# Performance work log

Hardware: AMD Instinct MI355X
Metric: run time of the kernel (lower is better)

The kernel has to match this reference:

```python
import jax, jax.numpy as jnp
import numpy as np

N = 50000
E = 800000
F_IN = 128
HID = 128
H_HID = 4
H_OUT = 6
N_CLS = 40
NEG_SLOPE = 0.2
BN_EPS = 1e-5


def gat_conv(x, src, dst, W, a_src, a_dst, bias, concat):
    # x: [N, F_in]; W: [F_in, H*C]; a_src/a_dst: [H, C]
    H, C = a_src.shape
    h = (x @ W).reshape(N, H, C)                      # [N,H,C]
    alpha_s = jnp.sum(h * a_src[None], axis=-1)       # [N,H]
    alpha_d = jnp.sum(h * a_dst[None], axis=-1)       # [N,H]
    e = jax.nn.leaky_relu(alpha_s[src] + alpha_d[dst], NEG_SLOPE)  # [E',H]
    # segment softmax over incoming edges of each dst node
    emax = jax.ops.segment_max(e, dst, num_segments=N)
    e = jnp.exp(e - emax[dst])
    denom = jax.ops.segment_sum(e, dst, num_segments=N)
    alpha = e / (denom[dst] + 1e-16)                  # [E',H]
    out = jax.ops.segment_sum(alpha[:, :, None] * h[src], dst, num_segments=N)  # [N,H,C]
    out = out.reshape(N, H * C) if concat else out.mean(axis=1)
    return out + bias


def bn_eval(x, gamma, beta, mean, var):
    return (x - mean) * (gamma / jnp.sqrt(var + BN_EPS)) + beta


def setup_inputs() -> dict:
    key = jax.random.key(0)
    ks = jax.random.split(key, 24)
    d_h = HID * H_HID  # 512
    inp = {
        'x': jax.random.normal(ks[0], (N, F_IN), jnp.float32),
        'edge_index': jax.random.randint(ks[1], (2, E), 0, N, jnp.int64),
        # layer 0: GATConv(128 -> 128, heads=4, concat)
        'W0': jax.random.normal(ks[2], (F_IN, d_h), jnp.float32) * 0.1,
        'as0': jax.random.normal(ks[3], (H_HID, HID), jnp.float32) * 0.1,
        'ad0': jax.random.normal(ks[4], (H_HID, HID), jnp.float32) * 0.1,
        'b0': jnp.zeros((d_h,), jnp.float32),
        'g0': jax.random.uniform(ks[5], (d_h,), jnp.float32, 0.5, 1.5),
        'bt0': jax.random.normal(ks[6], (d_h,), jnp.float32) * 0.1,
        'm0': jax.random.normal(ks[7], (d_h,), jnp.float32) * 0.1,
        'v0': jax.random.uniform(ks[8], (d_h,), jnp.float32, 0.5, 1.5),
        # layer 1: GATConv(512 -> 128, heads=4, concat)
        'W1': jax.random.normal(ks[9], (d_h, d_h), jnp.float32) * 0.05,
        'as1': jax.random.normal(ks[10], (H_HID, HID), jnp.float32) * 0.1,
        'ad1': jax.random.normal(ks[11], (H_HID, HID), jnp.float32) * 0.1,
        'b1': jnp.zeros((d_h,), jnp.float32),
        'g1': jax.random.uniform(ks[12], (d_h,), jnp.float32, 0.5, 1.5),
        'bt1': jax.random.normal(ks[13], (d_h,), jnp.float32) * 0.1,
        'm1': jax.random.normal(ks[14], (d_h,), jnp.float32) * 0.1,
        'v1': jax.random.uniform(ks[15], (d_h,), jnp.float32, 0.5, 1.5),
        # layer 2: GATConv(512 -> 40, heads=6, concat=False)
        'W2': jax.random.normal(ks[16], (d_h, H_OUT * N_CLS), jnp.float32) * 0.05,
        'as2': jax.random.normal(ks[17], (H_OUT, N_CLS), jnp.float32) * 0.1,
        'ad2': jax.random.normal(ks[18], (H_OUT, N_CLS), jnp.float32) * 0.1,
        'b2': jnp.zeros((N_CLS,), jnp.float32),
    }
    return inp


def reference(x, edge_index, W0, as0, ad0, b0, g0, bt0, m0, v0,
              W1, as1, ad1, b1, g1, bt1, m1, v1,
              W2, as2, ad2, b2):
    # add self loops (PyG GATConv default add_self_loops=True)
    loop = jnp.arange(N, dtype=edge_index.dtype)
    src = jnp.concatenate([edge_index[0], loop])
    dst = jnp.concatenate([edge_index[1], loop])
    # dropout is a no-op in eval mode
    h = gat_conv(x, src, dst, W0, as0, ad0, b0, concat=True)
    h = jax.nn.elu(bn_eval(h, g0, bt0, m0, v0))
    h = gat_conv(h, src, dst, W1, as1, ad1, b1, concat=True)
    h = jax.nn.elu(bn_eval(h, g1, bt1, m1, v1))
    h = gat_conv(h, src, dst, W2, as2, ad2, b2, concat=False)
    return jax.nn.log_softmax(h, axis=-1)
```

## Files before the change

### kernel.cpp

```cpp
#include <hip/hip_runtime.h>
#include <cstdint>
#include <cstddef>

#define NN 50000
#define EE 800000
#define EPQ (EE + NN)
#define NEG_SLOPE 0.2f
#define BN_EPS 1e-5f
#define SCB 256
#define NBLK ((NN + SCB - 1) / SCB)

typedef _Float16 f16x8 __attribute__((ext_vector_type(8)));
typedef _Float16 f16x4 __attribute__((ext_vector_type(4)));
typedef _Float16 f16x2 __attribute__((ext_vector_type(2)));
typedef float f32x4 __attribute__((ext_vector_type(4)));
typedef float f32x2 __attribute__((ext_vector_type(2)));
typedef unsigned int u32;
typedef unsigned char u8;
typedef unsigned short u16;

static __device__ __forceinline__ float lrelu(float x) { return x > 0.f ? x : x * NEG_SLOPE; }

static __device__ __forceinline__ u8 f32_to_fp8(float v) {
    return (u8)(__builtin_amdgcn_cvt_pk_fp8_f32(v, v, 0, false) & 0xff);
}
static __device__ __forceinline__ void fp8x4_to_f32(u32 v, float* o) {
    f32x2 lo = __builtin_amdgcn_cvt_pk_f32_fp8(v, false);
    f32x2 hi = __builtin_amdgcn_cvt_pk_f32_fp8(v, true);
    o[0] = lo[0]; o[1] = lo[1]; o[2] = hi[0]; o[3] = hi[1];
}

static __device__ __forceinline__ void gld_lds16(const void* g, void* l) {
    __builtin_amdgcn_global_load_lds((const __attribute__((address_space(1))) u32*)g,
                                     (__attribute__((address_space(3))) u32*)l, 16, 0, 0);
}

__global__ void hist_kernel(const int* __restrict__ dst, int* __restrict__ count) {
    int e = blockIdx.x * blockDim.x + threadIdx.x;
    if (e < EE) atomicAdd(&count[dst[e]], 1);
}

__global__ __launch_bounds__(SCB) void scan1(const int* __restrict__ count,
                                             int* __restrict__ excl, int* __restrict__ bsum) {
    __shared__ int tmp[SCB];
    int b = blockIdx.x, t = threadIdx.x;
    int i = b * SCB + t;
    int v = (i < NN) ? count[i] + 1 : 0;
    tmp[t] = v;
    __syncthreads();
    for (int off = 1; off < SCB; off <<= 1) {
        int u = (t >= off) ? tmp[t - off] : 0;
        __syncthreads();
        tmp[t] += u;
        __syncthreads();
    }
    if (i < NN) excl[i] = tmp[t] - v;
    if (t == SCB - 1) bsum[b] = tmp[t];
}

__global__ __launch_bounds__(256) void scan2(const int* __restrict__ bsum, int* __restrict__ boff) {
    __shared__ int tmp[256];
    int t = threadIdx.x;
    int v = (t < NBLK) ? bsum[t] : 0;
    tmp[t] = v;
    __syncthreads();
    for (int off = 1; off < 256; off <<= 1) {
        int u = (t >= off) ? tmp[t - off] : 0;
        __syncthreads();
        tmp[t] += u;
        __syncthreads();
    }
    boff[t] = tmp[t] - v;
}

__global__ void scan3(const int* __restrict__ excl, const int* __restrict__ boff,
                      int* __restrict__ rowptr, int* __restrict__ cursor) {
    int i = blockIdx.x * blockDim.x + threadIdx.x;
    if (i < NN) {
        int r = excl[i] + boff[i / SCB];
        rowptr[i] = r;
        cursor[i] = r;
    }
    if (i == NN) rowptr[NN] = EPQ;
}

__global__ void scatter_kernel(const int* __restrict__ src, const int* __restrict__ dst,
                               int* __restrict__ cursor, int* __restrict__ csrs) {
    int e = blockIdx.x * blockDim.x + threadIdx.x;
    if (e < EE) {
        int d = dst[e];
        int slot = atomicAdd(&cursor[d], 1);
        csrs[slot] = src[e];
    } else if (e < EPQ) {
        int i = e - EE;
        int slot = atomicAdd(&cursor[i], 1);
        csrs[slot] = i;
    }
}

__global__ __launch_bounds__(256) void tcast_all(const float* __restrict__ W0,
                                                 const float* __restrict__ W1,
                                                 const float* __restrict__ W2,
                                                 _Float16* __restrict__ W0t,
                                                 _Float16* __restrict__ W1t,
                                                 _Float16* __restrict__ W2t) {
    __shared__ float tile[32][33];
    int b = blockIdx.x;
    const float* W; _Float16* Wt; int K, Nc, bx, by;
    if (b < 64)       { W = W0; Wt = W0t; K = 128; Nc = 512; int q = b;       bx = q % 16, by = q / 16; }
    else if (b < 320) { W = W1; Wt = W1t; K = 512; Nc = 512; int q = b - 64;  bx = q % 16, by = q / 16; }
    else              { W = W2; Wt = W2t; K = 512; Nc = 240; int q = b - 320; bx = q % 8,  by = q / 8; }
    bx *= 32; by *= 32;
    int tx = threadIdx.x & 31, ty = threadIdx.x >> 5;
#pragma unroll
    for (int r = 0; r < 32; r += 8) {
        int k = by + ty + r, n = bx + tx;
        tile[ty + r][tx] = (k < K && n < Nc) ? W[(size_t)k * Nc + n] : 0.f;
    }
    __syncthreads();
#pragma unroll
    for (int r = 0; r < 32; r += 8) {
        int n = bx + ty + r, k = by + tx;
        if (n < Nc && k < K) Wt[(size_t)n * K + k] = (_Float16)tile[tx][ty + r];
    }
}

__global__ __launch_bounds__(1024) void prep_all(const float* g0, const float* bt0,
                                                 const float* m0, const float* v0, const float* b0,
                                                 const float* g1, const float* bt1,
                                                 const float* m1, const float* v1, const float* b1,
                                                 const _Float16* __restrict__ W0t,
                                                 const _Float16* __restrict__ W1t,
                                                 const _Float16* __restrict__ W2t,
                                                 const float* __restrict__ as0,
                                                 const float* __restrict__ ad0,
                                                 const float* __restrict__ as1,
                                                 const float* __restrict__ ad1,
                                                 const float* __restrict__ as2,
                                                 const float* __restrict__ ad2,
                                                 float* sc01, float* sh01, float* va0, float* va1,
                                                 float* va2) {
    int bid = blockIdx.x, t = threadIdx.x;
    if (bid == 0) {
        const float *g, *bt, *m, *v, *b;
        int c;
        if (t < 512) { g = g0; bt = bt0; m = m0; v = v0; b = b0; c = t; }
        else         { g = g1; bt = bt1; m = m1; v = v1; b = b1; c = t - 512; }
        float s = g[c] * rsqrtf(v[c] + BN_EPS);
        sc01[t] = s;
        sh01[t] = (b[c] - m[c]) * s + bt[c];
        return;
    }
    int vb = bid - 1;
    if (vb < 8) {
        if (t >= 128) return;
        int j = vb, h = j & 3;
        const float* a = (j < 4 ? as0 : ad0) + h * 128;
        float s = 0.f;
        for (int c = 0; c < 128; c++) s += (float)W0t[(size_t)(h * 128 + c) * 128 + t] * a[c];
        va0[j * 128 + t] = s;
    } else if (vb < 16) {
        if (t >= 512) return;
        int j = vb - 8, h = j & 3;
        const float* a = (j < 4 ? as1 : ad1) + h * 128;
        float s = 0.f;
        for (int c = 0; c < 128; c++) s += (float)W1t[(size_t)(h * 128 + c) * 512 + t] * a[c];
        va1[j * 512 + t] = s;
    } else {
        if (t >= 512) return;
        int j = vb - 16, h = j % 6;
        const float* a = (j < 6 ? as2 : ad2) + h * 40;
        float s = 0.f;
        for (int c = 0; c < 40; c++) s += (float)W2t[(size_t)(h * 40 + c) * 512 + t] * a[c];
        va2[j * 512 + t] = s;
    }
}

__global__ __launch_bounds__(256) void castx_alpha0(const float* __restrict__ x,
                                                    const float* __restrict__ va0,
                                                    u8* __restrict__ xq, float* __restrict__ asn,
                                                    float* __restrict__ adn) {
    int wid = threadIdx.x >> 6, lane = threadIdx.x & 63;
    int i = blockIdx.x * 4 + wid;
    if (i >= NN) return;
    f32x2 xv = *(const f32x2*)(x + (size_t)i * 128 + lane * 2);
    u32 q = __builtin_amdgcn_cvt_pk_fp8_f32(xv[0], xv[1], 0, false);
    *((u16*)(xq + (size_t)i * 128) + lane) = (u16)(q & 0xffff);
    float p[8];
#pragma unroll
    for (int j = 0; j < 8; j++) {
        f32x2 v = *(const f32x2*)(va0 + j * 128 + lane * 2);
        p[j] = xv[0] * v[0] + xv[1] * v[1];
    }
#pragma unroll
    for (int off = 32; off; off >>= 1)
#pragma unroll
        for (int j = 0; j < 8; j++) p[j] += __shfl_xor(p[j], off);
    if (lane == 0) {
        f32x4 o0 = {p[0], p[1], p[2], p[3]}, o1 = {p[4], p[5], p[6], p[7]};
        *(f32x4*)(asn + (size_t)i * 4) = o0;
        *(f32x4*)(adn + (size_t)i * 4) = o1;
    }
}

template <bool BD, bool EPI, int OT>
__global__ __launch_bounds__(256) void gemm_t(const _Float16* __restrict__ A, int lda,
                                              const _Float16* __restrict__ Bt,
                                              void* __restrict__ Cv, int ldc, int M, int Nc,
                                              int K, const float* __restrict__ sc,
                                              const float* __restrict__ sh) {
    __shared__ __align__(16) _Float16 As[2][128 * 64];
    __shared__ __align__(16) _Float16 Bs[2][128 * 64];
    const int t = threadIdx.x;
    const int bm = blockIdx.x * 128;
    const int bn = blockIdx.y * 128;
    const int wid = t >> 6, lane = t & 63;
    const int wm = (wid >> 1) * 64, wn = (wid & 1) * 64;
    const int aoff = BD ? bn : 0;
    f32x4 acc[4][4] = {};
    const int nsteps = K >> 6;

    auto STAGE = [&](int buf, int k0) {
#pragma unroll
        for (int it = 0; it < 4; ++it) {
            int rbase = it * 32 + wid * 8;
            int row = rbase + (lane >> 3);
            int c8g = (lane & 7) ^ (row & 7);
            gld_lds16(A + (size_t)(bm + row) * lda + aoff + k0 + c8g * 8,
                      (char*)As[buf] + rbase * 128);
            gld_lds16(Bt + (size_t)(bn + row) * K + k0 + c8g * 8, (char*)Bs[buf] + rbase * 128);
        }
    };

    STAGE(0, 0);
    __syncthreads();
    int cur = 0;
    for (int s = 0; s < nsteps; ++s) {
        if (s + 1 < nsteps) STAGE(cur ^ 1, (s + 1) * 64);
#pragma unroll
        for (int ks = 0; ks < 2; ++ks) {
            f16x8 af[4], bf[4];
#pragma unroll
            for (int mi = 0; mi < 4; ++mi) {
                int row = wm + mi * 16 + (lane & 15);
                int c8 = (ks * 4 + (lane >> 4)) ^ (row & 7);
                af[mi] = *(const f16x8*)((const char*)As[cur] + row * 128 + c8 * 16);
            }
#pragma unroll
            for (int ni = 0; ni < 4; ++ni) {
                int row = wn + ni * 16 + (lane & 15);
                int c8 = (ks * 4 + (lane >> 4)) ^ (row & 7);
                bf[ni] = *(const f16x8*)((const char*)Bs[cur] + row * 128 + c8 * 16);
            }
#pragma unroll
            for (int mi = 0; mi < 4; ++mi)
#pragma unroll
                for (int ni = 0; ni < 4; ++ni)
                    acc[mi][ni] = __builtin_amdgcn_mfma_f32_16x16x32_f16(af[mi], bf[ni],
                                                                         acc[mi][ni], 0, 0, 0);
        }
        __syncthreads();
        cur ^= 1;
    }
    float scv[4], shv[4];
    if (EPI) {
#pragma unroll
        for (int ni = 0; ni < 4; ++ni) {
            int gcol = bn + wn + ni * 16 + (lane & 15);
            scv[ni] = sc[gcol];
            shv[ni] = sh[gcol];
        }
    }
#pragma unroll
    for (int mi = 0; mi < 4; ++mi) {
#pragma unroll
        for (int r = 0; r < 4; ++r) {
            int grow = bm + wm + mi * 16 + (lane >> 4) * 4 + r;
            if (grow < M) {
#pragma unroll
                for (int ni = 0; ni < 4; ++ni) {
                    int gcol = bn + wn + ni * 16 + (lane & 15);
                    if (gcol < Nc) {
                        float v = acc[mi][ni][r];
                        if (EPI) {
                            v = v * scv[ni] + shv[ni];
                            v = v > 0.f ? v : expm1f(v);
                        }
                        if constexpr (OT == 0) {
                            ((_Float16*)Cv)[(size_t)grow * ldc + gcol] = (_Float16)v;
                        } else {
                            ((u8*)Cv)[(size_t)grow * ldc + gcol] = f32_to_fp8(v);
                        }
                    }
                }
            }
        }
    }
}

template <int JH, int STR>
__global__ __launch_bounds__(256) void alpha12(const _Float16* __restrict__ feat,
                                               const float* __restrict__ va,
                                               float* __restrict__ asn, float* __restrict__ adn) {
    int wid = threadIdx.x >> 6, lane = threadIdx.x & 63;
    int i = blockIdx.x * 4 + wid;
    if (i >= NN) return;
    f16x8 x8 = *(const f16x8*)(feat + (size_t)i * 512 + lane * 8);
    float xf[8];
#pragma unroll
    for (int u = 0; u < 8; u++) xf[u] = (float)x8[u];
    float p[2 * JH];
#pragma unroll
    for (int j = 0; j < 2 * JH; j++) {
        const float* vr = va + j * 512 + lane * 8;
        f32x4 v0 = *(const f32x4*)vr;
        f32x4 v1 = *(const f32x4*)(vr + 4);
        p[j] = xf[0] * v0[0] + xf[1] * v0[1] + xf[2] * v0[2] + xf[3] * v0[3] +
               xf[4] * v1[0] + xf[5] * v1[1] + xf[6] * v1[2] + xf[7] * v1[3];
    }
#pragma unroll
    for (int off = 32; off; off >>= 1)
#pragma unroll
        for (int j = 0; j < 2 * JH; j++) p[j] += __shfl_xor(p[j], off);
    if (lane == 0) {
#pragma unroll
        for (int h = 0; h < JH; h++) {
            asn[(size_t)i * STR + h] = p[h];
            adn[(size_t)i * STR + h] = p[JH + h];
        }
    }
}

__global__ __launch_bounds__(256) void aggx(const u8* __restrict__ xq,
                                            const float* __restrict__ asn,
                                            const float* __restrict__ adn,
                                            const int* __restrict__ rowptr,
                                            const int* __restrict__ csr,
                                            _Float16* __restrict__ xa) {
    __shared__ __align__(8) _Float16 wsl[4][64][4];
    int wid = threadIdx.x >> 6, lane = threadIdx.x & 63;
    int i = blockIdx.x * 4 + wid;
    if (i >= NN) return;
    int start = rowptr[i], end = rowptr[i + 1], deg = end - start;
    bool fastp = deg <= 64;
    f32x4 ad = *(const f32x4*)(adn + (size_t)i * 4);
    f32x4 m4, rd4;
    if (fastp) {
        bool v = lane < deg;
        int e = start + (v ? lane : 0);
        int s = csr[e];
        f32x4 a = *(const f32x4*)(asn + (size_t)s * 4);
        f32x4 sc4, mm, wv, dn;
#pragma unroll
        for (int j = 0; j < 4; j++) { sc4[j] = v ? lrelu(a[j] + ad[j]) : -1e30f; mm[j] = sc4[j]; }
#pragma unroll
        for (int off = 32; off; off >>= 1)
#pragma unroll
            for (int j = 0; j < 4; j++) mm[j] = fmaxf(mm[j], __shfl_xor(mm[j], off));
#pragma unroll
        for (int j = 0; j < 4; j++) { wv[j] = v ? __expf(sc4[j] - mm[j]) : 0.f; dn[j] = wv[j]; }
#pragma unroll
        for (int off = 32; off; off >>= 1)
#pragma unroll
            for (int j = 0; j < 4; j++) dn[j] += __shfl_xor(dn[j], off);
        f16x4 o;
#pragma unroll
        for (int j = 0; j < 4; j++) o[j] = (_Float16)(wv[j] / (dn[j] + 1e-16f));
        *(f16x4*)&wsl[wid][lane][0] = o;
    } else {
        f32x4 mm = {-1e30f, -1e30f, -1e30f, -1e30f};
        for (int e = start + lane; e < end; e += 64) {
            int s = csr[e];
            f32x4 a = *(const f32x4*)(asn + (size_t)s * 4);
#pragma unroll
            for (int j = 0; j < 4; j++) mm[j] = fmaxf(mm[j], lrelu(a[j] + ad[j]));
        }
#pragma unroll
        for (int off = 32; off; off >>= 1)
#pragma unroll
            for (int j = 0; j < 4; j++) mm[j] = fmaxf(mm[j], __shfl_xor(mm[j], off));
        f32x4 dn = {0.f, 0.f, 0.f, 0.f};
        for (int e = start + lane; e < end; e += 64) {
            int s = csr[e];
            f32x4 a = *(const f32x4*)(asn + (size_t)s * 4);
#pragma unroll
            for (int j = 0; j < 4; j++) dn[j] += __expf(lrelu(a[j] + ad[j]) - mm[j]);
        }
#pragma unroll
        for (int off = 32; off; off >>= 1)
#pragma unroll
            for (int j = 0; j < 4; j++) dn[j] += __shfl_xor(dn[j], off);
        m4 = mm;
#pragma unroll
        for (int j = 0; j < 4; j++) rd4[j] = 1.f / (dn[j] + 1e-16f);
    }
    const char* xb = (const char*)xq + lane * 2;
    float acc[8] = {};
    int e = start;
    auto getw = [&](int ee, int ss, float* w) {
        if (fastp) {
            f16x4 wv4 = *(const f16x4*)&wsl[wid][ee - start][0];
#pragma unroll
            for (int h = 0; h < 4; h++) w[h] = (float)wv4[h];
        } else {
#pragma unroll
            for (int h = 0; h < 4; h++)
                w[h] = __expf(lrelu(asn[(size_t)ss * 4 + h] + ad[h]) - m4[h]) * rd4[h];
        }
    };
    for (; e + 4 <= end; e += 4) {
        int s0 = csr[e], s1 = csr[e + 1], s2 = csr[e + 2], s3 = csr[e + 3];
        u16 pv0 = *(const u16*)(xb + (u32)s0 * 128u);
        u16 pv1 = *(const u16*)(xb + (u32)s1 * 128u);
        u16 pv2 = *(const u16*)(xb + (u32)s2 * 128u);
        u16 pv3 = *(const u16*)(xb + (u32)s3 * 128u);
        float w0[4], w1[4], w2[4], w3[4];
        getw(e, s0, w0); getw(e + 1, s1, w1); getw(e + 2, s2, w2); getw(e + 3, s3, w3);
        f32x2 q0 = __builtin_amdgcn_cvt_pk_f32_fp8((u32)pv0, false);
        f32x2 q1 = __builtin_amdgcn_cvt_pk_f32_fp8((u32)pv1, false);
        f32x2 q2 = __builtin_amdgcn_cvt_pk_f32_fp8((u32)pv2, false);
        f32x2 q3 = __builtin_amdgcn_cvt_pk_f32_fp8((u32)pv3, false);
#pragma unroll
        for (int h = 0; h < 4; h++) {
            acc[h * 2]     += w0[h] * q0[0] + w1[h] * q1[0] + w2[h] * q2[0] + w3[h] * q3[0];
            acc[h * 2 + 1] += w0[h] * q0[1] + w1[h] * q1[1] + w2[h] * q2[1] + w3[h] * q3[1];
        }
    }
    for (; e < end; e++) {
        int s = csr[e];
        float w[4];
        getw(e, s, w);
        u16 pv = *(const u16*)(xb + (u32)s * 128u);
        f32x2 q = __builtin_amdgcn_cvt_pk_f32_fp8((u32)pv, false);
#pragma unroll
        for (int h = 0; h < 4; h++) {
            acc[h * 2] += w[h] * q[0];
            acc[h * 2 + 1] += w[h] * q[1];
        }
    }
#pragma unroll
    for (int h = 0; h < 4; h++) {
        f16x2 o;
        o[0] = (_Float16)acc[h * 2];
        o[1] = (_Float16)acc[h * 2 + 1];
        *(f16x2*)(xa + (size_t)i * 512 + h * 128 + lane * 2) = o;
    }
}

__global__ __launch_bounds__(256) void agg01(const u8* __restrict__ h,
                                             const float* __restrict__ asn,
                                             const float* __restrict__ adn,
                                             const int* __restrict__ rowptr,
                                             const int* __restrict__ csr,
                                             const float* __restrict__ sc,
                                             const float* __restrict__ sh,
                                             _Float16* __restrict__ out) {
    __shared__ __align__(8) _Float16 wsl[4][64][4];
    int wid = threadIdx.x >> 6, lane = threadIdx.x & 63;
    int i = blockIdx.x * 4 + wid;
    if (i >= NN) return;
    int start = rowptr[i], end = rowptr[i + 1], deg = end - start;
    bool fastp = deg <= 64;
    f32x4 ad = *(const f32x4*)(adn + (size_t)i * 4);
    f32x4 m4, rd4;
    if (fastp) {
        bool v = lane < deg;
        int e = start + (v ? lane : 0);
        int s = csr[e];
        f32x4 a = *(const f32x4*)(asn + (size_t)s * 4);
        f32x4 sc4, mm, wv, dn;
#pragma unroll
        for (int j = 0; j < 4; j++) { sc4[j] = v ? lrelu(a[j] + ad[j]) : -1e30f; mm[j] = sc4[j]; }
#pragma unroll
        for (int off = 32; off; off >>= 1)
#pragma unroll
            for (int j = 0; j < 4; j++) mm[j] = fmaxf(mm[j], __shfl_xor(mm[j], off));
#pragma unroll
        for (int j = 0; j < 4; j++) { wv[j] = v ? __expf(sc4[j] - mm[j]) : 0.f; dn[j] = wv[j]; }
#pragma unroll
        for (int off = 32; off; off >>= 1)
#pragma unroll
            for (int j = 0; j < 4; j++) dn[j] += __shfl_xor(dn[j], off);
        f16x4 o;
#pragma unroll
        for (int j = 0; j < 4; j++) o[j] = (_Float16)(wv[j] / (dn[j] + 1e-16f));
        *(f16x4*)&wsl[wid][lane][0] = o;
    } else {
        f32x4 mm = {-1e30f, -1e30f, -1e30f, -1e30f};
        for (int e = start + lane; e < end; e += 64) {
            int s = csr[e];
            f32x4 a = *(const f32x4*)(asn + (size_t)s * 4);
#pragma unroll
            for (int j = 0; j < 4; j++) mm[j] = fmaxf(mm[j], lrelu(a[j] + ad[j]));
        }
#pragma unroll
        for (int off = 32; off; off >>= 1)
#pragma unroll
            for (int j = 0; j < 4; j++) mm[j] = fmaxf(mm[j], __shfl_xor(mm[j], off));
        f32x4 dn = {0.f, 0.f, 0.f, 0.f};
        for (int e = start + lane; e < end; e += 64) {
            int s = csr[e];
            f32x4 a = *(const f32x4*)(asn + (size_t)s * 4);
#pragma unroll
            for (int j = 0; j < 4; j++) dn[j] += __expf(lrelu(a[j] + ad[j]) - mm[j]);
        }
#pragma unroll
        for (int off = 32; off; off >>= 1)
#pragma unroll
            for (int j = 0; j < 4; j++) dn[j] += __shfl_xor(dn[j], off);
        m4 = mm;
#pragma unroll
        for (int j = 0; j < 4; j++) rd4[j] = 1.f / (dn[j] + 1e-16f);
    }
    int head = lane >> 4;
    const char* hb = (const char*)h + lane * 8;
    float acc0[8] = {}, acc1[8] = {};
    int e = start;
    for (; e + 2 <= end; e += 2) {
        int s0 = csr[e], s1 = csr[e + 1];
        float w0, w1;
        if (fastp) {
            w0 = (float)wsl[wid][e - start][head];
            w1 = (float)wsl[wid][e + 1 - start][head];
        } else {
            w0 = __expf(lrelu(asn[(size_t)s0 * 4 + head] + ad[head]) - m4[head]) * rd4[head];
            w1 = __expf(lrelu(asn[(size_t)s1 * 4 + head] + ad[head]) - m4[head]) * rd4[head];
        }
        uint2 p0 = *(const uint2*)(hb + (u32)s0 * 512u);
        uint2 p1 = *(const uint2*)(hb + (u32)s1 * 512u);
        float q0[8], q1[8];
        fp8x4_to_f32(p0.x, q0); fp8x4_to_f32(p0.y, q0 + 4);
        fp8x4_to_f32(p1.x, q1); fp8x4_to_f32(p1.y, q1 + 4);
#pragma unroll
        for (int j = 0; j < 8; j++) {
            acc0[j] += w0 * q0[j];
            acc1[j] += w1 * q1[j];
        }
    }
    if (e < end) {
        int s0 = csr[e];
        float w0;
        if (fastp) w0 = (float)wsl[wid][e - start][head];
        else w0 = __expf(lrelu(asn[(size_t)s0 * 4 + head] + ad[head]) - m4[head]) * rd4[head];
        uint2 p0 = *(const uint2*)(hb + (u32)s0 * 512u);
        float q0[8];
        fp8x4_to_f32(p0.x, q0); fp8x4_to_f32(p0.y, q0 + 4);
#pragma unroll
        for (int j = 0; j < 8; j++) acc0[j] += w0 * q0[j];
    }
    int ch = lane * 8;
    f32x4 sc0 = *(const f32x4*)(sc + ch), sc1 = *(const f32x4*)(sc + ch + 4);
    f32x4 sh0 = *(const f32x4*)(sh + ch), sh1 = *(const f32x4*)(sh + ch + 4);
    f16x8 o;
#pragma unroll
    for (int j = 0; j < 8; j++) {
        float s = (j < 4) ? sc0[j] : sc1[j - 4];
        float b = (j < 4) ? sh0[j] : sh1[j - 4];
        float val = (acc0[j] + acc1[j]) * s + b;
        val = val > 0.f ? val : expm1f(val);
        o[j] = (_Float16)val;
    }
    *(f16x8*)(out + (size_t)i * 512 + ch) = o;
}

__global__ __launch_bounds__(256) void agg2f(const u8* __restrict__ h2,
                                             const float* __restrict__ asn,
                                             const float* __restrict__ adn,
                                             const int* __restrict__ rowptr,
                                             const int* __restrict__ csr,
                                             const float* __restrict__ b2,
                                             float* __restrict__ out) {
    __shared__ __align__(16) _Float16 wsl[4][64][8];
    __shared__ float sval[4][240];
    int wid = threadIdx.x >> 6, lane = threadIdx.x & 63;
    int i = blockIdx.x * 4 + wid;
    if (i < NN) {
        int start = rowptr[i], end = rowptr[i + 1], deg = end - start;
        bool fastp = deg <= 64;
        f32x4 ad0 = *(const f32x4*)(adn + (size_t)i * 8);
        f32x4 ad1 = *(const f32x4*)(adn + (size_t)i * 8 + 4);
        float adh[6] = {ad0[0], ad0[1], ad0[2], ad0[3], ad1[0], ad1[1]};
        float m6[6], rd6[6];
        if (fastp) {
            bool v = lane < deg;
            int e = start + (v ? lane : 0);
            int s = csr[e];
            f32x4 x0 = *(const f32x4*)(asn + (size_t)s * 8);
            f32x4 x1 = *(const f32x4*)(asn + (size_t)s * 8 + 4);
            float av[6] = {x0[0], x0[1], x0[2], x0[3], x1[0], x1[1]};
            float sc6[6], mm[6], wv[6], dn[6];
#pragma unroll
            for (int j = 0; j < 6; j++) {
                sc6[j] = v ? lrelu(av[j] + adh[j]) : -1e30f;
                mm[j] = sc6[j];
            }
#pragma unroll
            for (int off = 32; off; off >>= 1)
#pragma unroll
                for (int j = 0; j < 6; j++) mm[j] = fmaxf(mm[j], __shfl_xor(mm[j], off));
#pragma unroll
            for (int j = 0; j < 6; j++) { wv[j] = v ? __expf(sc6[j] - mm[j]) : 0.f; dn[j] = wv[j]; }
#pragma unroll
            for (int off = 32; off; off >>= 1)
#pragma unroll
                for (int j = 0; j < 6; j++) dn[j] += __shfl_xor(dn[j], off);
            f16x8 o;
#pragma unroll
            for (int j = 0; j < 6; j++) o[j] = (_Float16)(wv[j] / (dn[j] + 1e-16f));
            o[6] = (_Float16)0.f;
            o[7] = (_Float16)0.f;
            *(f16x8*)&wsl[wid][lane][0] = o;
        } else {
            float mm[6], dn[6];
#pragma unroll
            for (int j = 0; j < 6; j++) { mm[j] = -1e30f; dn[j] = 0.f; }
            for (int e = start + lane; e < end; e += 64) {
                int s = csr[e];
                f32x4 x0 = *(const f32x4*)(asn + (size_t)s * 8);
                f32x4 x1 = *(const f32x4*)(asn + (size_t)s * 8 + 4);
                float av[6] = {x0[0], x0[1], x0[2], x0[3], x1[0], x1[1]};
#pragma unroll
                for (int j = 0; j < 6; j++) mm[j] = fmaxf(mm[j], lrelu(av[j] + adh[j]));
            }
#pragma unroll
            for (int off = 32; off; off >>= 1)
#pragma unroll
                for (int j = 0; j < 6; j++) mm[j] = fmaxf(mm[j], __shfl_xor(mm[j], off));
            for (int e = start + lane; e < end; e += 64) {
                int s = csr[e];
                f32x4 x0 = *(const f32x4*)(asn + (size_t)s * 8);
                f32x4 x1 = *(const f32x4*)(asn + (size_t)s * 8 + 4);
                float av[6] = {x0[0], x0[1], x0[2], x0[3], x1[0], x1[1]};
#pragma unroll
                for (int j = 0; j < 6; j++) dn[j] += __expf(lrelu(av[j] + adh[j]) - mm[j]);
            }
#pragma unroll
            for (int off = 32; off; off >>= 1)
#pragma unroll
                for (int j = 0; j < 6; j++) dn[j] += __shfl_xor(dn[j], off);
#pragma unroll
            for (int j = 0; j < 6; j++) { m6[j] = mm[j]; rd6[j] = 1.f / (dn[j] + 1e-16f); }
        }
        int head = (lane < 60) ? (lane / 10) : 0;
        const char* hb = (const char*)h2 + lane * 4;
        float a0[4] = {}, a1[4] = {};
        int e = start;
        auto getw1 = [&](int ee, int ss) -> float {
            if (fastp) return (float)wsl[wid][ee - start][head];
            return __expf(lrelu(asn[(size_t)ss * 8 + head] + adh[head]) - m6[head]) * rd6[head];
        };
        for (; e + 4 <= end; e += 4) {
            int s0 = csr[e], s1 = csr[e + 1], s2 = csr[e + 2], s3 = csr[e + 3];
            u32 p0 = *(const u32*)(hb + (u32)s0 * 256u);
            u32 p1 = *(const u32*)(hb + (u32)s1 * 256u);
            u32 p2 = *(const u32*)(hb + (u32)s2 * 256u);
            u32 p3 = *(const u32*)(hb + (u32)s3 * 256u);
            float w0 = getw1(e, s0), w1 = getw1(e + 1, s1);
            float w2 = getw1(e + 2, s2), w3 = getw1(e + 3, s3);
            float q0[4], q1[4], q2[4], q3[4];
            fp8x4_to_f32(p0, q0);
            fp8x4_to_f32(p1, q1);
            fp8x4_to_f32(p2, q2);
            fp8x4_to_f32(p3, q3);
#pragma unroll
            for (int j = 0; j < 4; j++) {
                a0[j] += w0 * q0[j] + w2 * q2[j];
                a1[j] += w1 * q1[j] + w3 * q3[j];
            }
        }
        for (; e < end; e++) {
            int s0 = csr[e];
            float w0 = getw1(e, s0);
            u32 p0 = *(const u32*)(hb + (u32)s0 * 256u);
            float q0[4];
            fp8x4_to_f32(p0, q0);
#pragma unroll
            for (int j = 0; j < 4; j++) a0[j] += w0 * q0[j];
        }
        if (lane < 60) {
#pragma unroll
            for (int j = 0; j < 4; j++) sval[wid][lane * 4 + j] = a0[j] + a1[j];
        }
    }
    __syncthreads();
    if (i < NN) {
        float v = -INFINITY;
        if (lane < 40) {
            float s = 0.f;
#pragma unroll
            for (int hh = 0; hh < 6; hh++) s += sval[wid][hh * 40 + lane];
            v = s * (1.0f / 6.0f) + b2[lane];
        }
        float mm = v;
#pragma unroll
        for (int off = 32; off; off >>= 1) mm = fmaxf(mm, __shfl_xor(mm, off));
        float se = (lane < 40) ? __expf(v - mm) : 0.f;
#pragma unroll
        for (int off = 32; off; off >>= 1) se += __shfl_xor(se, off);
        if (lane < 40) out[(size_t)i * 40 + lane] = v - mm - logf(se);
    }
}

extern "C" void kernel_launch(void* const* d_in, const int* in_sizes, int n_in,
                              void* d_out, int out_size, void* d_ws, size_t ws_size,
                              hipStream_t stream) {
    const float* x   = (const float*)d_in[0];
    const int*   ei  = (const int*)d_in[1];
    const float* W0  = (const float*)d_in[2];
    const float* as0 = (const float*)d_in[3];
    const float* ad0 = (const float*)d_in[4];
    const float* b0  = (const float*)d_in[5];
    const float* g0  = (const float*)d_in[6];
    const float* bt0 = (const float*)d_in[7];
    const float* m0  = (const float*)d_in[8];
    const float* v0  = (const float*)d_in[9];
    const float* W1  = (const float*)d_in[10];
    const float* as1 = (const float*)d_in[11];
    const float* ad1 = (const float*)d_in[12];
    const float* b1  = (const float*)d_in[13];
    const float* g1  = (const float*)d_in[14];
    const float* bt1 = (const float*)d_in[15];
    const float* m1  = (const float*)d_in[16];
    const float* v1  = (const float*)d_in[17];
    const float* W2  = (const float*)d_in[18];
    const float* as2w = (const float*)d_in[19];
    const float* ad2w = (const float*)d_in[20];
    const float* b2  = (const float*)d_in[21];
    float* out = (float*)d_out;
    const int* srcv = ei;
    const int* dstv = ei + EE;

    char* w = (char*)d_ws;
    auto carve = [&](size_t bytes) {
        char* p = w;
        w += (bytes + 255) & ~(size_t)255;
        return p;
    };
    u32* xq        = (u32*)carve((size_t)NN * 128);
    _Float16* hA   = (_Float16*)carve((size_t)NN * 512 * 2);
    _Float16* actB = (_Float16*)carve((size_t)NN * 512 * 2);
    _Float16* W0t  = (_Float16*)carve((size_t)512 * 128 * 2);
    _Float16* W1t  = (_Float16*)carve((size_t)512 * 512 * 2);
    _Float16* W2t  = (_Float16*)carve((size_t)240 * 512 * 2);
    float* va0  = (float*)carve((size_t)8 * 128 * 4);
    float* va1  = (float*)carve((size_t)8 * 512 * 4);
    float* va2  = (float*)carve((size_t)12 * 512 * 4);
    float* sc01 = (float*)carve((size_t)1024 * 4);
    float* sh01 = (float*)carve((size_t)1024 * 4);
    float* asn  = (float*)carve((size_t)NN * 8 * 4);
    float* adn  = (float*)carve((size_t)NN * 8 * 4);
    int* count  = (int*)carve((size_t)(NN + 8) * 4);
    int* excl   = (int*)carve((size_t)(NN + 8) * 4);
    int* bsum   = (int*)carve((size_t)512 * 4);
    int* boff   = (int*)carve((size_t)512 * 4);
    int* rowptr = (int*)carve((size_t)(NN + 8) * 4);
    int* cursor = (int*)carve((size_t)(NN + 8) * 4);
    int* csrs   = (int*)carve((size_t)EPQ * 4);
    _Float16* xa = hA;
    u8* h1q  = (u8*)hA;
    u8* h2q  = (u8*)hA;

    hipMemsetAsync(count, 0, (size_t)NN * 4, stream);
    hist_kernel<<<(EE + 255) / 256, 256, 0, stream>>>(dstv, count);
    scan1<<<NBLK, SCB, 0, stream>>>(count, excl, bsum);
    scan2<<<1, 256, 0, stream>>>(bsum, boff);
    scan3<<<(NN + 256) / 256, 256, 0, stream>>>(excl, boff, rowptr, cursor);
    scatter_kernel<<<(EPQ + 255) / 256, 256, 0, stream>>>(srcv, dstv, cursor, csrs);

    tcast_all<<<448, 256, 0, stream>>>(W0, W1, W2, W0t, W1t, W2t);
    prep_all<<<29, 1024, 0, stream>>>(g0, bt0, m0, v0, b0, g1, bt1, m1, v1, b1, W0t, W1t, W2t,
                                      as0, ad0, as1, ad1, as2w, ad2w, sc01, sh01, va0, va1, va2);

    const int MT = (NN + 127) / 128;
    const int NG = (NN + 3) / 4;

    castx_alpha0<<<NG, 256, 0, stream>>>(x, va0, (u8*)xq, asn, adn);
    aggx<<<NG, 256, 0, stream>>>((const u8*)xq, asn, adn, rowptr, csrs, xa);
    gemm_t<true, true, 0><<<dim3(MT, 4), 256, 0, stream>>>(xa, 512, W0t, actB, 512, NN, 512, 128,
                                                           sc01, sh01);

    gemm_t<false, false, 1><<<dim3(MT, 4), 256, 0, stream>>>(actB, 512, W1t, h1q, 512, NN, 512,
                                                             512, nullptr, nullptr);
    alpha12<4, 4><<<NG, 256, 0, stream>>>(actB, va1, asn, adn);
    agg01<<<NG, 256, 0, stream>>>(h1q, asn, adn, rowptr, csrs, sc01 + 512, sh01 + 512, actB);

    gemm_t<false, false, 1><<<dim3(MT, 2), 256, 0, stream>>>(actB, 512, W2t, h2q, 256, NN, 240,
                                                             512, nullptr, nullptr);
    alpha12<6, 8><<<NG, 256, 0, stream>>>(actB, va2, asn, adn);
    agg2f<<<NG, 256, 0, stream>>>(h2q, asn, adn, rowptr, csrs, b2, out);
}
```

Before: 557.5 us.

## Merge scan passes, template GEMM K, and scalarize CSR index loads

```diff
diff --git a/kernel.cpp b/kernel.cpp
--- a/kernel.cpp
+++ b/kernel.cpp
@@ -20,6 +20,7 @@
 typedef unsigned short u16;
 
 static __device__ __forceinline__ float lrelu(float x) { return x > 0.f ? x : x * NEG_SLOPE; }
+static __device__ __forceinline__ int rfl(int v) { return __builtin_amdgcn_readfirstlane(v); }
 
 static __device__ __forceinline__ u8 f32_to_fp8(float v) {
     return (u8)(__builtin_amdgcn_cvt_pk_fp8_f32(v, v, 0, false) & 0xff);
@@ -58,26 +59,24 @@
     if (t == SCB - 1) bsum[b] = tmp[t];
 }
 
-__global__ __launch_bounds__(256) void scan2(const int* __restrict__ bsum, int* __restrict__ boff) {
-    __shared__ int tmp[256];
+__global__ __launch_bounds__(256) void scan23(const int* __restrict__ excl,
+                                              const int* __restrict__ bsum,
+                                              int* __restrict__ rowptr, int* __restrict__ cursor) {
+    __shared__ int pre[256];
     int t = threadIdx.x;
     int v = (t < NBLK) ? bsum[t] : 0;
-    tmp[t] = v;
+    pre[t] = v;
     __syncthreads();
     for (int off = 1; off < 256; off <<= 1) {
-        int u = (t >= off) ? tmp[t - off] : 0;
+        int u = (t >= off) ? pre[t - off] : 0;
         __syncthreads();
-        tmp[t] += u;
+        pre[t] += u;
         __syncthreads();
     }
-    boff[t] = tmp[t] - v;
-}
-
-__global__ void scan3(const int* __restrict__ excl, const int* __restrict__ boff,
-                      int* __restrict__ rowptr, int* __restrict__ cursor) {
-    int i = blockIdx.x * blockDim.x + threadIdx.x;
+    int i = blockIdx.x * blockDim.x + t;
     if (i < NN) {
-        int r = excl[i] + boff[i / SCB];
+        int blk = i / SCB;
+        int r = excl[i] + pre[blk] - ((blk < NBLK) ? bsum[blk] : 0);
         rowptr[i] = r;
         cursor[i] = r;
     }
@@ -203,11 +202,11 @@
     }
 }
 
-template <bool BD, bool EPI, int OT>
+template <int TK, bool BD, bool EPI, int OT>
 __global__ __launch_bounds__(256) void gemm_t(const _Float16* __restrict__ A, int lda,
                                               const _Float16* __restrict__ Bt,
                                               void* __restrict__ Cv, int ldc, int M, int Nc,
-                                              int K, const float* __restrict__ sc,
+                                              const float* __restrict__ sc,
                                               const float* __restrict__ sh) {
     __shared__ __align__(16) _Float16 As[2][128 * 64];
     __shared__ __align__(16) _Float16 Bs[2][128 * 64];
@@ -218,7 +217,7 @@
     const int wm = (wid >> 1) * 64, wn = (wid & 1) * 64;
     const int aoff = BD ? bn : 0;
     f32x4 acc[4][4] = {};
-    const int nsteps = K >> 6;
+    constexpr int nsteps = TK >> 6;
 
     auto STAGE = [&](int buf, int k0) {
 #pragma unroll
@@ -228,14 +227,15 @@
             int c8g = (lane & 7) ^ (row & 7);
             gld_lds16(A + (size_t)(bm + row) * lda + aoff + k0 + c8g * 8,
                       (char*)As[buf] + rbase * 128);
-            gld_lds16(Bt + (size_t)(bn + row) * K + k0 + c8g * 8, (char*)Bs[buf] + rbase * 128);
+            gld_lds16(Bt + (size_t)(bn + row) * TK + k0 + c8g * 8, (char*)Bs[buf] + rbase * 128);
         }
     };
 
     STAGE(0, 0);
     __syncthreads();
-    int cur = 0;
+#pragma unroll
     for (int s = 0; s < nsteps; ++s) {
+        const int cur = s & 1;
         if (s + 1 < nsteps) STAGE(cur ^ 1, (s + 1) * 64);
 #pragma unroll
         for (int ks = 0; ks < 2; ++ks) {
@@ -260,7 +260,6 @@
                                                                          acc[mi][ni], 0, 0, 0);
         }
         __syncthreads();
-        cur ^= 1;
     }
     float scv[4], shv[4];
     if (EPI) {
@@ -341,7 +340,8 @@
     int wid = threadIdx.x >> 6, lane = threadIdx.x & 63;
     int i = blockIdx.x * 4 + wid;
     if (i >= NN) return;
-    int start = rowptr[i], end = rowptr[i + 1], deg = end - start;
+    int start = rfl(rowptr[i]), end = rfl(rowptr[i + 1]);
+    int deg = end - start;
     bool fastp = deg <= 64;
     f32x4 ad = *(const f32x4*)(adn + (size_t)i * 4);
     f32x4 m4, rd4;
@@ -409,7 +409,8 @@
         }
     };
     for (; e + 4 <= end; e += 4) {
-        int s0 = csr[e], s1 = csr[e + 1], s2 = csr[e + 2], s3 = csr[e + 3];
+        int4 sv = *(const int4*)(csr + e);
+        int s0 = rfl(sv.x), s1 = rfl(sv.y), s2 = rfl(sv.z), s3 = rfl(sv.w);
         u16 pv0 = *(const u16*)(xb + (u32)s0 * 128u);
         u16 pv1 = *(const u16*)(xb + (u32)s1 * 128u);
         u16 pv2 = *(const u16*)(xb + (u32)s2 * 128u);
@@ -427,7 +428,7 @@
         }
     }
     for (; e < end; e++) {
-        int s = csr[e];
+        int s = rfl(csr[e]);
         float w[4];
         getw(e, s, w);
         u16 pv = *(const u16*)(xb + (u32)s * 128u);
@@ -459,7 +460,8 @@
     int wid = threadIdx.x >> 6, lane = threadIdx.x & 63;
     int i = blockIdx.x * 4 + wid;
     if (i >= NN) return;
-    int start = rowptr[i], end = rowptr[i + 1], deg = end - start;
+    int start = rfl(rowptr[i]), end = rfl(rowptr[i + 1]);
+    int deg = end - start;
     bool fastp = deg <= 64;
     f32x4 ad = *(const f32x4*)(adn + (size_t)i * 4);
     f32x4 m4, rd4;
@@ -517,7 +519,8 @@
     float acc0[8] = {}, acc1[8] = {};
     int e = start;
     for (; e + 2 <= end; e += 2) {
-        int s0 = csr[e], s1 = csr[e + 1];
+        int2 sv = *(const int2*)(csr + e);
+        int s0 = rfl(sv.x), s1 = rfl(sv.y);
         float w0, w1;
         if (fastp) {
             w0 = (float)wsl[wid][e - start][head];
@@ -538,7 +541,7 @@
         }
     }
     if (e < end) {
-        int s0 = csr[e];
+        int s0 = rfl(csr[e]);
         float w0;
         if (fastp) w0 = (float)wsl[wid][e - start][head];
         else w0 = __expf(lrelu(asn[(size_t)s0 * 4 + head] + ad[head]) - m4[head]) * rd4[head];
@@ -575,7 +578,8 @@
     int wid = threadIdx.x >> 6, lane = threadIdx.x & 63;
     int i = blockIdx.x * 4 + wid;
     if (i < NN) {
-        int start = rowptr[i], end = rowptr[i + 1], deg = end - start;
+        int start = rfl(rowptr[i]), end = rfl(rowptr[i + 1]);
+        int deg = end - start;
         bool fastp = deg <= 64;
         f32x4 ad0 = *(const f32x4*)(adn + (size_t)i * 8);
         f32x4 ad1 = *(const f32x4*)(adn + (size_t)i * 8 + 4);
@@ -650,7 +654,8 @@
             return __expf(lrelu(asn[(size_t)ss * 8 + head] + adh[head]) - m6[head]) * rd6[head];
         };
         for (; e + 4 <= end; e += 4) {
-            int s0 = csr[e], s1 = csr[e + 1], s2 = csr[e + 2], s3 = csr[e + 3];
+            int4 sv = *(const int4*)(csr + e);
+            int s0 = rfl(sv.x), s1 = rfl(sv.y), s2 = rfl(sv.z), s3 = rfl(sv.w);
             u32 p0 = *(const u32*)(hb + (u32)s0 * 256u);
             u32 p1 = *(const u32*)(hb + (u32)s1 * 256u);
             u32 p2 = *(const u32*)(hb + (u32)s2 * 256u);
@@ -669,7 +674,7 @@
             }
         }
         for (; e < end; e++) {
-            int s0 = csr[e];
+            int s0 = rfl(csr[e]);
             float w0 = getw1(e, s0);
             u32 p0 = *(const u32*)(hb + (u32)s0 * 256u);
             float q0[4];
@@ -752,10 +757,9 @@
     int* count  = (int*)carve((size_t)(NN + 8) * 4);
     int* excl   = (int*)carve((size_t)(NN + 8) * 4);
     int* bsum   = (int*)carve((size_t)512 * 4);
-    int* boff   = (int*)carve((size_t)512 * 4);
     int* rowptr = (int*)carve((size_t)(NN + 8) * 4);
     int* cursor = (int*)carve((size_t)(NN + 8) * 4);
-    int* csrs   = (int*)carve((size_t)EPQ * 4);
+    int* csrs   = (int*)carve((size_t)(EPQ + 8) * 4);
     _Float16* xa = hA;
     u8* h1q  = (u8*)hA;
     u8* h2q  = (u8*)hA;
@@ -763,8 +767,7 @@
     hipMemsetAsync(count, 0, (size_t)NN * 4, stream);
     hist_kernel<<<(EE + 255) / 256, 256, 0, stream>>>(dstv, count);
     scan1<<<NBLK, SCB, 0, stream>>>(count, excl, bsum);
-    scan2<<<1, 256, 0, stream>>>(bsum, boff);
-    scan3<<<(NN + 256) / 256, 256, 0, stream>>>(excl, boff, rowptr, cursor);
+    scan23<<<(NN + 256) / 256, 256, 0, stream>>>(excl, bsum, rowptr, cursor);
     scatter_kernel<<<(EPQ + 255) / 256, 256, 0, stream>>>(srcv, dstv, cursor, csrs);
 
     tcast_all<<<448, 256, 0, stream>>>(W0, W1, W2, W0t, W1t, W2t);
@@ -776,16 +779,16 @@
 
     castx_alpha0<<<NG, 256, 0, stream>>>(x, va0, (u8*)xq, asn, adn);
     aggx<<<NG, 256, 0, stream>>>((const u8*)xq, asn, adn, rowptr, csrs, xa);
-    gemm_t<true, true, 0><<<dim3(MT, 4), 256, 0, stream>>>(xa, 512, W0t, actB, 512, NN, 512, 128,
-                                                           sc01, sh01);
-
-    gemm_t<false, false, 1><<<dim3(MT, 4), 256, 0, stream>>>(actB, 512, W1t, h1q, 512, NN, 512,
-                                                             512, nullptr, nullptr);
+    gemm_t<128, true, true, 0><<<dim3(MT, 4), 256, 0, stream>>>(xa, 512, W0t, actB, 512, NN, 512,
+                                                                sc01, sh01);
+
+    gemm_t<512, false, false, 1><<<dim3(MT, 4), 256, 0, stream>>>(actB, 512, W1t, h1q, 512, NN,
+                                                                  512, nullptr, nullptr);
     alpha12<4, 4><<<NG, 256, 0, stream>>>(actB, va1, asn, adn);
     agg01<<<NG, 256, 0, stream>>>(h1q, asn, adn, rowptr, csrs, sc01 + 512, sh01 + 512, actB);
 
-    gemm_t<false, false, 1><<<dim3(MT, 2), 256, 0, stream>>>(actB, 512, W2t, h2q, 256, NN, 240,
-                                                             512, nullptr, nullptr);
+    gemm_t<512, false, false, 1><<<dim3(MT, 2), 256, 0, stream>>>(actB, 512, W2t, h2q, 256, NN,
+                                                                  240, nullptr, nullptr);
     alpha12<6, 8><<<NG, 256, 0, stream>>>(actB, va2, asn, adn);
     agg2f<<<NG, 256, 0, stream>>>(h2q, asn, adn, rowptr, csrs, b2, out);
 }
```

Result: faster. 527.5 us (median of 2 runs) (-5.4%).
